# Kernel optimization log

Hardware: AMD Instinct MI355X
Metric: run time of the kernel (lower is better)

## Reference

```python
import jax, jax.numpy as jnp
import numpy as np


def conv3d(x, w, b, pad):
    # x: (B,C,D,H,W), w: (O,I,kd,kh,kw)
    y = jax.lax.conv_general_dilated(
        x, w, window_strides=(1, 1, 1), padding=[(pad, pad)] * 3,
        dimension_numbers=('NCDHW', 'OIDHW', 'NCDHW'))
    return y + b[None, :, None, None, None]


def setup_inputs() -> dict:
    key = jax.random.key(0)
    ks = jax.random.split(key, 8)
    B, C, D, H, W = 8, 128, 16, 32, 32
    C8 = C // 8
    return {
        'x': jax.random.normal(ks[0], (B, C, D, H, W), dtype=jnp.float32),
        'gamma': jax.random.normal(ks[1], (1,), dtype=jnp.float32),
        'w_k': jax.random.normal(ks[2], (C8, C, 1, 1, 1), dtype=jnp.float32) * 0.05,
        'b_k': jax.random.normal(ks[3], (C8,), dtype=jnp.float32) * 0.05,
        'w_q': jax.random.normal(ks[4], (C8, C, 1, 1, 1), dtype=jnp.float32) * 0.05,
        'b_q': jax.random.normal(ks[5], (C8,), dtype=jnp.float32) * 0.05,
        'w_v': jax.random.normal(ks[6], (C, C, 3, 3, 3), dtype=jnp.float32) * 0.02,
        'b_v': jax.random.normal(ks[7], (C,), dtype=jnp.float32) * 0.05,
    }


def reference(x, gamma, w_k, b_k, w_q, b_q, w_v, b_v):
    B, C, D, H, W = x.shape
    HW = H * W
    k = conv3d(x, w_k, b_k, 0)   # (B, C/8, D, H, W)
    q = conv3d(x, w_q, b_q, 0)   # (B, C/8, D, H, W)
    v = conv3d(x, w_v, b_v, 1)   # (B, C, D, H, W)

    # --- spatial (P) attention over HW positions, feature dim (C/8)*D ---
    kf = k.reshape(B, -1, HW)
    qf = q.reshape(B, -1, HW)
    # cor[b,s,t] = sum_f k[b,f,s] q[b,f,t]; softmax over t
    A_p = jax.nn.softmax(jnp.einsum('bfs,bft->bst', kf, qf), axis=-1)  # (B,HW,HW)
    vf = v.reshape(B, C * D, HW)
    # Patt[b,m,j] = sum_t v[b,m,t] A_p[b,j,t]  (v @ A_p^T)
    Patt = jnp.einsum('bmt,bjt->bmj', vf, A_p).reshape(B, C, D, H, W)

    # --- depth (D) attention over D slices, feature dim (C/8)*H*W ---
    kd = k.transpose(0, 2, 1, 3, 4).reshape(B, D, -1)
    qd = q.transpose(0, 2, 1, 3, 4).reshape(B, D, -1)
    A_d = jax.nn.softmax(jnp.einsum('bdf,bef->bde', kd, qd), axis=-1)  # (B,D,D)
    vd = v.transpose(0, 2, 1, 3, 4).reshape(B, D, -1)  # (B, D, C*H*W)
    # Datt[b,j,f] = sum_d A_d[b,j,d] vd[b,d,f]
    Datt = jnp.einsum('bjd,bdf->bjf', A_d, vd).reshape(B, D, C, H, W)
    Datt = Datt.transpose(0, 2, 1, 3, 4)  # (B,C,D,H,W)

    return gamma[0] * (Patt + Datt) + x
```

## Files before the change

kernel.cpp:

```cpp
#include <hip/hip_runtime.h>

#define HW   1024
#define DHW  16384

typedef __attribute__((ext_vector_type(8))) short short8;
typedef __attribute__((ext_vector_type(4))) float f32x4;

static __device__ __forceinline__ ushort f2bf(float f) {
  unsigned u = __float_as_uint(f);
  unsigned r = (u + 0x7fffu + ((u >> 16) & 1u)) >> 16;
  return (ushort)r;
}
static __device__ __forceinline__ float bf2f(ushort u) {
  return __uint_as_float(((unsigned)u) << 16);
}
static __device__ __forceinline__ void async_copy16(const ushort* g, ushort* l) {
  __builtin_amdgcn_global_load_lds(
      (const __attribute__((address_space(1))) unsigned int*)g,
      (__attribute__((address_space(3))) unsigned int*)l, 16, 0, 0);
}

__global__ __launch_bounds__(256) void kq_kernel(
    const float* __restrict__ x, const float* __restrict__ wk,
    const float* __restrict__ bk, const float* __restrict__ wq,
    const float* __restrict__ bq, float* __restrict__ k, float* __restrict__ q,
    ushort* __restrict__ xt) {
  __shared__ float wks[16 * 128];
  __shared__ float wqs[16 * 128];
  int tid = threadIdx.x;
  for (int i = tid; i < 2048; i += 256) { wks[i] = wk[i]; wqs[i] = wq[i]; }
  __syncthreads();
  int b = blockIdx.y;
  int p = blockIdx.x * 256 + tid;
  int z = p >> 10, hw = p & 1023;
  float ak[16], aq[16];
#pragma unroll
  for (int o = 0; o < 16; ++o) { ak[o] = 0.f; aq[o] = 0.f; }
  const float* xb = x + (size_t)b * 128 * DHW + p;
  ushort* xtp = xt + (((size_t)(b * 16 + z) * 16) * 1024 + hw) * 8;
  for (int chunk = 0; chunk < 16; ++chunk) {
    ushort pack[8];
#pragma unroll
    for (int c8 = 0; c8 < 8; ++c8) {
      int c = chunk * 8 + c8;
      float xv = xb[(size_t)c * DHW];
      pack[c8] = f2bf(xv);
#pragma unroll
      for (int o = 0; o < 16; ++o) {
        ak[o] += wks[o * 128 + c] * xv;
        aq[o] += wqs[o * 128 + c] * xv;
      }
    }
    *(uint4*)&xtp[(size_t)chunk * 1024 * 8] = *(const uint4*)pack;
  }
#pragma unroll
  for (int o = 0; o < 16; ++o) {
    k[((size_t)b * 16 + o) * DHW + p] = ak[o] + bk[o];
    q[((size_t)b * 16 + o) * DHW + p] = aq[o] + bq[o];
  }
}

__global__ __launch_bounds__(256) void wprep_kernel(
    const float* __restrict__ wv, ushort* __restrict__ wt,
    ushort* __restrict__ zbuf) {
  if (blockIdx.x == 0 && threadIdx.x < 512) zbuf[threadIdx.x] = 0;
  int i = blockIdx.x * 256 + threadIdx.x;
  if (i >= 27 * 128 * 128) return;
  int c8 = i & 7;
  int t = i >> 3;
  int o = t & 127; t >>= 7;
  int tap = t % 9; t /= 9;
  int chunk = t & 15;
  int kd = t >> 4;
  wt[i] = f2bf(wv[(size_t)(o * 128 + chunk * 8 + c8) * 27 + kd * 9 + tap]);
}

__global__ __launch_bounds__(256, 2) void vconv_mfma_kernel(
    const ushort* __restrict__ xt, const ushort* __restrict__ wt,
    const float* __restrict__ bv, const ushort* __restrict__ zbuf,
    ushort* __restrict__ v) {
  __shared__ __align__(16) ushort xs[1536 * 8];
  __shared__ __align__(16) ushort wsm[2304 * 8];
  int tid = threadIdx.x;
  int wave = tid >> 6;
  int ml = tid & 15;
  int quad = (tid >> 4) & 3;
  int bz = blockIdx.x;
  int b = bz & 7, z = bz >> 3;
  int h0 = blockIdx.y * 8;
  int o0 = blockIdx.z * 64;

  f32x4 acc[4][4];
#pragma unroll
  for (int s = 0; s < 4; ++s)
#pragma unroll
    for (int t = 0; t < 4; ++t) acc[s][t] = (f32x4){0.f, 0.f, 0.f, 0.f};

  int cb0[4];
#pragma unroll
  for (int t = 0; t < 4; ++t)
    cb0[t] = (wave * 2 + (t >> 1)) * 34 + (t & 1) * 16 + ml;

  int xoff[6]; bool okx[6];
#pragma unroll
  for (int it = 0; it < 6; ++it) {
    int i = it * 256 + tid;
    int cu = i / 340;
    int cell = i - cu * 340;
    int hr = cell / 34;
    int wc = cell - hr * 34;
    int h = h0 + hr - 1, ww = wc - 1;
    okx[it] = (i < 1360) && ((unsigned)h < 32u) && ((unsigned)ww < 32u);
    xoff[it] = cu * 1024 + h * 32 + ww;
  }
  int woff[9];
#pragma unroll
  for (int it = 0; it < 9; ++it) {
    int i = it * 256 + tid;
    int cu = i / 576;
    int r = i - cu * 576;
    int tap = r >> 6, ol = r & 63;
    woff[it] = (cu * 9 + tap) * 128 + o0 + ol;
  }

  const int KH[9] = {0, 0, 0, 1, 1, 1, 2, 2, 2};
  const int KW[9] = {0, 1, 2, 0, 1, 2, 0, 1, 2};

  for (int kd = 0; kd < 3; ++kd) {
    int zd = z + kd - 1;
    bool zok = (zd >= 0 && zd < 16);
    int zdc = zok ? zd : 0;
    const ushort* xbase = xt + (size_t)(b * 16 + zdc) * 16 * 1024 * 8;
    for (int cb = 0; cb < 4; ++cb) {
      const ushort* xsb = xbase + (size_t)cb * 4 * 1024 * 8;
      const ushort* wsb = wt + (size_t)(kd * 16 + cb * 4) * 9 * 128 * 8;
#pragma unroll
      for (int it = 0; it < 6; ++it) {
        const ushort* g = (zok && okx[it]) ? xsb + (size_t)xoff[it] * 8 : zbuf;
        async_copy16(g, &xs[(it * 256 + tid) * 8]);
      }
#pragma unroll
      for (int it = 0; it < 9; ++it)
        async_copy16(wsb + (size_t)woff[it] * 8, &wsm[(it * 256 + tid) * 8]);
      __syncthreads();
#pragma unroll
      for (int tap = 0; tap < 9; ++tap) {
        const int kh = KH[tap], kw = KW[tap];
        short8 af[4], bfr[4];
#pragma unroll
        for (int s = 0; s < 4; ++s)
          af[s] = *(const short8*)&wsm[(quad * 576 + tap * 64 + s * 16 + ml) * 8];
#pragma unroll
        for (int t = 0; t < 4; ++t) {
          int cell = cb0[t] + kh * 34 + kw;
          bfr[t] = *(const short8*)&xs[(quad * 340 + cell) * 8];
        }
#pragma unroll
        for (int s = 0; s < 4; ++s)
#pragma unroll
          for (int t = 0; t < 4; ++t)
            acc[s][t] = __builtin_amdgcn_mfma_f32_16x16x32_bf16(af[s], bfr[t], acc[s][t], 0, 0, 0);
      }
      __syncthreads();
    }
  }
#pragma unroll
  for (int s = 0; s < 4; ++s) {
    int o = o0 + s * 16 + quad * 4;
#pragma unroll
    for (int t = 0; t < 4; ++t) {
      int pl = wave * 64 + t * 16 + ml;
      ushort* dst = &v[((size_t)(b * 128 + o) * 16 + z) * 1024 + h0 * 32 + pl];
#pragma unroll
      for (int r = 0; r < 4; ++r)
        dst[(size_t)r * 16384] = f2bf(acc[s][t][r] + bv[o + r]);
    }
  }
}

__global__ __launch_bounds__(256) void kqt_kernel(
    const float* __restrict__ k, const float* __restrict__ q,
    ushort* __restrict__ kT, ushort* __restrict__ qT,
    float* __restrict__ rsum, float* __restrict__ Sd) {
  __shared__ __align__(16) ushort tile[32 * 264];
  int tid = threadIdx.x;
  int t0 = blockIdx.x;
  int b = blockIdx.y;
  if (t0 == 0) {
    *(float4*)&rsum[b * 1024 + tid * 4] = (float4){0.f, 0.f, 0.f, 0.f};
    Sd[b * 256 + tid] = 0.f;
  }
  int h0 = t0 * 32;

  {
    const float* s = k + (size_t)b * 16 * DHW;
    for (int it = 0; it < 32; ++it) {
      int i = it * 256 + tid;
      int oo = i >> 9, zz = (i >> 5) & 15, hl = i & 31;
      tile[hl * 264 + oo * 16 + zz] =
          f2bf(s[(size_t)oo * DHW + zz * 1024 + h0 + hl]);
    }
    __syncthreads();
    ushort* d = kT + ((size_t)b * 1024 + h0) * 256;
    for (int jt = 0; jt < 4; ++jt) {
      int j = jt * 256 + tid;
      int hl = j >> 5, c8 = (j & 31) * 8;
      *(uint4*)&d[(size_t)hl * 256 + c8] = *(const uint4*)&tile[hl * 264 + c8];
    }
    __syncthreads();
  }
  {
    const float* s = q + (size_t)b * 16 * DHW;
    for (int it = 0; it < 32; ++it) {
      int i = it * 256 + tid;
      int oo = i >> 9, zz = (i >> 5) & 15, hl = i & 31;
      tile[hl * 264 + oo * 16 + zz] =
          f2bf(s[(size_t)oo * DHW + zz * 1024 + h0 + hl]);
    }
    __syncthreads();
    ushort* d = qT + ((size_t)b * 1024 + h0) * 256;
    for (int jt = 0; jt < 4; ++jt) {
      int j = jt * 256 + tid;
      int hl = j >> 5, c8 = (j & 31) * 8;
      *(uint4*)&d[(size_t)hl * 256 + c8] = *(const uint4*)&tile[hl * 264 + c8];
    }
  }
}

__global__ __launch_bounds__(256, 2) void apx_kernel(
    const ushort* __restrict__ kT, const ushort* __restrict__ qT,
    ushort* __restrict__ A_p, float* __restrict__ rsum) {
  __shared__ __align__(16) ushort smem[32768];
  int tid = threadIdx.x;
  int wave = tid >> 6, lane = tid & 63;
  int ml = lane & 15, quad = lane >> 4;
  int wm = wave >> 1, wj = wave & 1;
  int b = blockIdx.x;
  int tile = blockIdx.y;
  int m0 = (tile >> 3) * 128;
  int j0 = (tile & 7) * 128;

  f32x4 acc[4][4];
#pragma unroll
  for (int s = 0; s < 4; ++s)
#pragma unroll
    for (int t = 0; t < 4; ++t) acc[s][t] = (f32x4){0.f, 0.f, 0.f, 0.f};

  const ushort* va = kT + ((size_t)b * 1024 + m0) * 256;
  const ushort* pa = qT + ((size_t)b * 1024 + j0) * 256;

  int srow[4], skc[4];
#pragma unroll
  for (int n = 0; n < 4; ++n) {
    int slot = wave * 256 + n * 64 + lane;
    srow[n] = slot >> 3;
    skc[n] = (slot & 7) ^ (srow[n] & 7);
  }

#pragma unroll
  for (int n = 0; n < 4; ++n) {
    async_copy16(va + (size_t)srow[n] * 256 + skc[n] * 8,
                 &smem[(wave * 256 + n * 64) * 8]);
    async_copy16(pa + (size_t)srow[n] * 256 + skc[n] * 8,
                 &smem[8192 + (wave * 256 + n * 64) * 8]);
  }
  __syncthreads();

  for (int t = 0; t < 4; ++t) {
    int cur = (t & 1) * 16384;
    int nxt = 16384 - cur;
    if (t < 3) {
      int kk = (t + 1) * 64;
#pragma unroll
      for (int n = 0; n < 4; ++n) {
        async_copy16(va + (size_t)srow[n] * 256 + kk + skc[n] * 8,
                     &smem[nxt + (wave * 256 + n * 64) * 8]);
        async_copy16(pa + (size_t)srow[n] * 256 + kk + skc[n] * 8,
                     &smem[nxt + 8192 + (wave * 256 + n * 64) * 8]);
      }
    }
#pragma unroll
    for (int ks = 0; ks < 2; ++ks) {
      short8 af[4], bfr[4];
#pragma unroll
      for (int s = 0; s < 4; ++s) {
        int row = wm * 64 + s * 16 + ml;
        int c = ks * 4 + quad;
        af[s] = *(const short8*)&smem[cur + (row * 8 + (c ^ (row & 7))) * 8];
      }
#pragma unroll
      for (int t2 = 0; t2 < 4; ++t2) {
        int row = wj * 64 + t2 * 16 + ml;
        int c = ks * 4 + quad;
        bfr[t2] = *(const short8*)&smem[cur + 8192 + (row * 8 + (c ^ (row & 7))) * 8];
      }
#pragma unroll
      for (int s = 0; s < 4; ++s)
#pragma unroll
        for (int t2 = 0; t2 < 4; ++t2)
          acc[s][t2] = __builtin_amdgcn_mfma_f32_16x16x32_bf16(af[s], bfr[t2], acc[s][t2], 0, 0, 0);
    }
    __syncthreads();
  }

#pragma unroll
  for (int s = 0; s < 4; ++s)
#pragma unroll
    for (int r = 0; r < 4; ++r) {
      float sum = 0.f;
#pragma unroll
      for (int t2 = 0; t2 < 4; ++t2) {
        float p = __expf(acc[s][t2][r]);
        acc[s][t2][r] = p;
        sum += p;
      }
      sum += __shfl_xor(sum, 1);
      sum += __shfl_xor(sum, 2);
      sum += __shfl_xor(sum, 4);
      sum += __shfl_xor(sum, 8);
      if (ml == 0) {
        int m = m0 + wm * 64 + s * 16 + quad * 4 + r;
        atomicAdd(&rsum[b * 1024 + m], sum);
      }
    }
#pragma unroll
  for (int s = 0; s < 4; ++s)
#pragma unroll
    for (int t2 = 0; t2 < 4; ++t2) {
      int j = j0 + wj * 64 + t2 * 16 + ml;
#pragma unroll
      for (int r = 0; r < 4; ++r) {
        int m = m0 + wm * 64 + s * 16 + quad * 4 + r;
        A_p[((size_t)b * 1024 + m) * 1024 + j] = f2bf(acc[s][t2][r]);
      }
    }
}

__global__ __launch_bounds__(256) void ad_part_kernel(
    const float* __restrict__ k, const float* __restrict__ q,
    float* __restrict__ Sd) {
  int tid = threadIdx.x;
  int b = blockIdx.x;
  int dj = blockIdx.y;
  int split = blockIdx.z;
  float acc[16];
#pragma unroll
  for (int e = 0; e < 16; ++e) acc[e] = 0.f;
  const float* kb = k + (size_t)b * 256 * HW;
  const float* qb = q + (size_t)b * 256 * HW;
  int fend = (split + 1) * 4096;
  for (int f = split * 4096 + tid; f < fend; f += 256) {
    int oc = f >> 10, hw = f & 1023;
    float kv = kb[(oc * 16 + dj) * HW + hw];
#pragma unroll
    for (int e = 0; e < 16; ++e)
      acc[e] += kv * qb[(oc * 16 + e) * HW + hw];
  }
  int lane = tid & 63;
#pragma unroll
  for (int e = 0; e < 16; ++e) {
    float s = acc[e];
    for (int off = 32; off >= 1; off >>= 1) s += __shfl_xor(s, off);
    if (lane == 0) atomicAdd(&Sd[b * 256 + dj * 16 + e], s);
  }
}

__global__ __launch_bounds__(128) void ad_fin_kernel(
    const float* __restrict__ Sd, float* __restrict__ A_d) {
  int t = threadIdx.x;
  const float* row = Sd + (size_t)t * 16;
  float m = row[0];
#pragma unroll
  for (int e = 1; e < 16; ++e) m = fmaxf(m, row[e]);
  float p[16], s = 0.f;
#pragma unroll
  for (int e = 0; e < 16; ++e) { p[e] = __expf(row[e] - m); s += p[e]; }
  float inv = 1.f / s;
#pragma unroll
  for (int e = 0; e < 16; ++e) A_d[(size_t)t * 16 + e] = p[e] * inv;
}

__global__ __launch_bounds__(256, 2) void combine_mfma_kernel(
    const ushort* __restrict__ vb, const ushort* __restrict__ apb,
    const float* __restrict__ A_d, const float* __restrict__ rsum,
    const float* __restrict__ x, const float* __restrict__ gamma,
    float* __restrict__ out) {
  __shared__ __align__(16) ushort smem[32768];
  __shared__ float Adt[272];
  int tid = threadIdx.x;
  int wave = tid >> 6, lane = tid & 63;
  int ml = lane & 15, quad = lane >> 4;
  int wm = wave >> 1, wj = wave & 1;
  int b = blockIdx.x;
  int tile = blockIdx.y;
  int m0 = (tile >> 3) * 128;
  int j0 = (tile & 7) * 128;
  Adt[(tid & 15) * 17 + (tid >> 4)] = A_d[b * 256 + tid];

  f32x4 acc[4][4];
#pragma unroll
  for (int s = 0; s < 4; ++s)
#pragma unroll
    for (int t = 0; t < 4; ++t) acc[s][t] = (f32x4){0.f, 0.f, 0.f, 0.f};

  const ushort* va = vb + ((size_t)b * 2048 + m0) * 1024;
  const ushort* pa = apb + ((size_t)b * 1024 + j0) * 1024;

  int srow[4], skc[4];
#pragma unroll
  for (int n = 0; n < 4; ++n) {
    int slot = wave * 256 + n * 64 + lane;
    srow[n] = slot >> 3;
    skc[n] = (slot & 7) ^ (srow[n] & 7);
  }

#pragma unroll
  for (int n = 0; n < 4; ++n) {
    async_copy16(va + (size_t)srow[n] * 1024 + skc[n] * 8,
                 &smem[(wave * 256 + n * 64) * 8]);
    async_copy16(pa + (size_t)srow[n] * 1024 + skc[n] * 8,
                 &smem[8192 + (wave * 256 + n * 64) * 8]);
  }
  __syncthreads();

  for (int t = 0; t < 16; ++t) {
    int cur = (t & 1) * 16384;
    int nxt = 16384 - cur;
    if (t < 15) {
      int kk = (t + 1) * 64;
#pragma unroll
      for (int n = 0; n < 4; ++n) {
        async_copy16(va + (size_t)srow[n] * 1024 + kk + skc[n] * 8,
                     &smem[nxt + (wave * 256 + n * 64) * 8]);
        async_copy16(pa + (size_t)srow[n] * 1024 + kk + skc[n] * 8,
                     &smem[nxt + 8192 + (wave * 256 + n * 64) * 8]);
      }
    }
#pragma unroll
    for (int ks = 0; ks < 2; ++ks) {
      short8 af[4], bfr[4];
#pragma unroll
      for (int s = 0; s < 4; ++s) {
        int row = wm * 64 + s * 16 + ml;
        int c = ks * 4 + quad;
        af[s] = *(const short8*)&smem[cur + (row * 8 + (c ^ (row & 7))) * 8];
      }
#pragma unroll
      for (int t2 = 0; t2 < 4; ++t2) {
        int row = wj * 64 + t2 * 16 + ml;
        int c = ks * 4 + quad;
        bfr[t2] = *(const short8*)&smem[cur + 8192 + (row * 8 + (c ^ (row & 7))) * 8];
      }
#pragma unroll
      for (int s = 0; s < 4; ++s)
#pragma unroll
        for (int t2 = 0; t2 < 4; ++t2)
          acc[s][t2] = __builtin_amdgcn_mfma_f32_16x16x32_bf16(af[s], bfr[t2], acc[s][t2], 0, 0, 0);
    }
    __syncthreads();
  }

  float invr[4];
#pragma unroll
  for (int t2 = 0; t2 < 4; ++t2)
    invr[t2] = 1.f / rsum[b * 1024 + j0 + wj * 64 + t2 * 16 + ml];
#pragma unroll
  for (int s = 0; s < 4; ++s)
#pragma unroll
    for (int t2 = 0; t2 < 4; ++t2)
#pragma unroll
      for (int r = 0; r < 4; ++r) acc[s][t2][r] *= invr[t2];

  for (int i = tid; i < 2048; i += 256) {
    int row = i >> 4, jc = i & 15;
    uint4 val = *(const uint4*)&vb[((size_t)b * 2048 + m0 + row) * 1024 + j0 + jc * 8];
    *(uint4*)&smem[row * 136 + jc * 8] = val;
  }
  __syncthreads();

#pragma unroll
  for (int d = 0; d < 16; ++d) {
    float ar[4];
#pragma unroll
    for (int r = 0; r < 4; ++r) ar[r] = Adt[d * 17 + quad * 4 + r];
#pragma unroll
    for (int s = 0; s < 4; ++s) {
      const ushort* vrow = &smem[(wm * 64 + s * 16 + d) * 136];
#pragma unroll
      for (int t2 = 0; t2 < 4; ++t2) {
        float vv = bf2f(vrow[wj * 64 + t2 * 16 + ml]);
#pragma unroll
        for (int r = 0; r < 4; ++r) acc[s][t2][r] += ar[r] * vv;
      }
    }
  }

  float g = gamma[0];
#pragma unroll
  for (int s = 0; s < 4; ++s) {
#pragma unroll
    for (int t2 = 0; t2 < 4; ++t2) {
      int jrel = wj * 64 + t2 * 16 + ml;
#pragma unroll
      for (int r = 0; r < 4; ++r) {
        int m = m0 + wm * 64 + s * 16 + quad * 4 + r;
        size_t idx = ((size_t)b * 2048 + m) * 1024 + j0 + jrel;
        out[idx] = g * acc[s][t2][r] + x[idx];
      }
    }
  }
}

extern "C" void kernel_launch(void* const* d_in, const int* in_sizes, int n_in,
                              void* d_out, int out_size, void* d_ws, size_t ws_size,
                              hipStream_t stream) {
  const float* x     = (const float*)d_in[0];
  const float* gamma = (const float*)d_in[1];
  const float* w_k   = (const float*)d_in[2];
  const float* b_k   = (const float*)d_in[3];
  const float* w_q   = (const float*)d_in[4];
  const float* b_q   = (const float*)d_in[5];
  const float* w_v   = (const float*)d_in[6];
  const float* b_v   = (const float*)d_in[7];
  float* out = (float*)d_out;

  float* k    = (float*)d_ws;
  float* q    = k + 2097152;
  float* A_d  = q + 2097152;
  ushort* vbf = (ushort*)(A_d + 2048);
  ushort* apb = vbf + 16777216;
  ushort* wt  = apb + 8388608;
  ushort* zbuf = wt + 442368;
  ushort* xt  = zbuf + 512;
  ushort* kT16 = xt;
  ushort* qT16 = xt + 2097152;
  float* rsum  = (float*)(xt + 4194304);
  float* Sd    = rsum + 8192;

  wprep_kernel<<<dim3(1728), 256, 0, stream>>>(w_v, wt, zbuf);
  kq_kernel<<<dim3(64, 8), 256, 0, stream>>>(x, w_k, b_k, w_q, b_q, k, q, xt);
  vconv_mfma_kernel<<<dim3(128, 4, 2), 256, 0, stream>>>(xt, wt, b_v, zbuf, vbf);
  kqt_kernel<<<dim3(32, 8), 256, 0, stream>>>(k, q, kT16, qT16, rsum, Sd);
  apx_kernel<<<dim3(8, 64), 256, 0, stream>>>(kT16, qT16, apb, rsum);
  ad_part_kernel<<<dim3(8, 16, 4), 256, 0, stream>>>(k, q, Sd);
  ad_fin_kernel<<<dim3(1), 128, 0, stream>>>(Sd, A_d);
  combine_mfma_kernel<<<dim3(8, 128), 256, 0, stream>>>(vbf, apb, A_d, rsum, x, gamma, out);
}
```

Baseline: 374.0 us.

## Merge small kernels to cut launch count and fold depth softmax into combine

Weight prep and the k/q projection now run in one launch, split by block index, and the kq weight smem layout is transposed so each channel's weights load as float4. The depth-attention partial sums run as extra blocks of the spatial attention kernel. The tiny depth softmax kernel is removed; each combine block recomputes the 16x16 softmax from Sd in shared memory. This removes several launches and serial gaps at the cost of redundant softmax work per block and mixed workloads within a grid. The Adt write by tid<16 relies on a later barrier in the main loop before Adt is read.

Result: faster. 333.2 us (-10.9%).

```diff
diff --git a/kernel.cpp b/kernel.cpp
--- a/kernel.cpp
+++ b/kernel.cpp
@@ -20,18 +20,37 @@
       (__attribute__((address_space(3))) unsigned int*)l, 16, 0, 0);
 }
 
-__global__ __launch_bounds__(256) void kq_kernel(
+__global__ __launch_bounds__(256) void prep_kernel(
     const float* __restrict__ x, const float* __restrict__ wk,
     const float* __restrict__ bk, const float* __restrict__ wq,
-    const float* __restrict__ bq, float* __restrict__ k, float* __restrict__ q,
-    ushort* __restrict__ xt) {
-  __shared__ float wks[16 * 128];
-  __shared__ float wqs[16 * 128];
+    const float* __restrict__ bq, const float* __restrict__ wv,
+    float* __restrict__ k, float* __restrict__ q,
+    ushort* __restrict__ xt, ushort* __restrict__ wt,
+    ushort* __restrict__ zbuf) {
+  __shared__ float wks[2048];
+  __shared__ float wqs[2048];
+  int gid = blockIdx.x;
   int tid = threadIdx.x;
-  for (int i = tid; i < 2048; i += 256) { wks[i] = wk[i]; wqs[i] = wq[i]; }
+  if (gid >= 512) {
+    if (gid == 512 && tid < 512) zbuf[tid] = 0;
+    int i = (gid - 512) * 256 + tid;
+    int c8 = i & 7;
+    int t = i >> 3;
+    int o = t & 127; t >>= 7;
+    int tap = t % 9; t /= 9;
+    int chunk = t & 15;
+    int kd = t >> 4;
+    wt[i] = f2bf(wv[(size_t)(o * 128 + chunk * 8 + c8) * 27 + kd * 9 + tap]);
+    return;
+  }
+  for (int i = tid; i < 2048; i += 256) {
+    int c = i >> 4, o = i & 15;
+    wks[i] = wk[o * 128 + c];
+    wqs[i] = wq[o * 128 + c];
+  }
   __syncthreads();
-  int b = blockIdx.y;
-  int p = blockIdx.x * 256 + tid;
+  int b = gid >> 6, bx = gid & 63;
+  int p = bx * 256 + tid;
   int z = p >> 10, hw = p & 1023;
   float ak[16], aq[16];
 #pragma unroll
@@ -45,10 +64,15 @@
       int c = chunk * 8 + c8;
       float xv = xb[(size_t)c * DHW];
       pack[c8] = f2bf(xv);
-#pragma unroll
-      for (int o = 0; o < 16; ++o) {
-        ak[o] += wks[o * 128 + c] * xv;
-        aq[o] += wqs[o * 128 + c] * xv;
+      const float4* wkc = (const float4*)&wks[c * 16];
+      const float4* wqc = (const float4*)&wqs[c * 16];
+#pragma unroll
+      for (int g = 0; g < 4; ++g) {
+        float4 wa = wkc[g], wb = wqc[g];
+        ak[g * 4 + 0] += wa.x * xv; ak[g * 4 + 1] += wa.y * xv;
+        ak[g * 4 + 2] += wa.z * xv; ak[g * 4 + 3] += wa.w * xv;
+        aq[g * 4 + 0] += wb.x * xv; aq[g * 4 + 1] += wb.y * xv;
+        aq[g * 4 + 2] += wb.z * xv; aq[g * 4 + 3] += wb.w * xv;
       }
     }
     *(uint4*)&xtp[(size_t)chunk * 1024 * 8] = *(const uint4*)pack;
@@ -58,21 +82,6 @@
     k[((size_t)b * 16 + o) * DHW + p] = ak[o] + bk[o];
     q[((size_t)b * 16 + o) * DHW + p] = aq[o] + bq[o];
   }
-}
-
-__global__ __launch_bounds__(256) void wprep_kernel(
-    const float* __restrict__ wv, ushort* __restrict__ wt,
-    ushort* __restrict__ zbuf) {
-  if (blockIdx.x == 0 && threadIdx.x < 512) zbuf[threadIdx.x] = 0;
-  int i = blockIdx.x * 256 + threadIdx.x;
-  if (i >= 27 * 128 * 128) return;
-  int c8 = i & 7;
-  int t = i >> 3;
-  int o = t & 127; t >>= 7;
-  int tap = t % 9; t /= 9;
-  int chunk = t & 15;
-  int kd = t >> 4;
-  wt[i] = f2bf(wv[(size_t)(o * 128 + chunk * 8 + c8) * 27 + kd * 9 + tap]);
 }
 
 __global__ __launch_bounds__(256, 2) void vconv_mfma_kernel(
@@ -227,16 +236,46 @@
   }
 }
 
-__global__ __launch_bounds__(256, 2) void apx_kernel(
+__global__ __launch_bounds__(256, 2) void att_kernel(
     const ushort* __restrict__ kT, const ushort* __restrict__ qT,
-    ushort* __restrict__ A_p, float* __restrict__ rsum) {
+    ushort* __restrict__ A_p, float* __restrict__ rsum,
+    const float* __restrict__ k, const float* __restrict__ q,
+    float* __restrict__ Sd) {
   __shared__ __align__(16) ushort smem[32768];
   int tid = threadIdx.x;
+  int b = blockIdx.x;
+  int by = blockIdx.y;
+
+  if (by >= 64) {
+    int t = by - 64;
+    int dj = t & 15, split = t >> 4;
+    float acc[16];
+#pragma unroll
+    for (int e = 0; e < 16; ++e) acc[e] = 0.f;
+    const float* kb = k + (size_t)b * 256 * HW;
+    const float* qb = q + (size_t)b * 256 * HW;
+    int fend = (split + 1) * 4096;
+    for (int f = split * 4096 + tid; f < fend; f += 256) {
+      int oc = f >> 10, hw = f & 1023;
+      float kv = kb[(oc * 16 + dj) * HW + hw];
+#pragma unroll
+      for (int e = 0; e < 16; ++e)
+        acc[e] += kv * qb[(oc * 16 + e) * HW + hw];
+    }
+    int lane = tid & 63;
+#pragma unroll
+    for (int e = 0; e < 16; ++e) {
+      float s = acc[e];
+      for (int off = 32; off >= 1; off >>= 1) s += __shfl_xor(s, off);
+      if (lane == 0) atomicAdd(&Sd[b * 256 + dj * 16 + e], s);
+    }
+    return;
+  }
+
   int wave = tid >> 6, lane = tid & 63;
   int ml = lane & 15, quad = lane >> 4;
   int wm = wave >> 1, wj = wave & 1;
-  int b = blockIdx.x;
-  int tile = blockIdx.y;
+  int tile = by;
   int m0 = (tile >> 3) * 128;
   int j0 = (tile & 7) * 128;
 
@@ -336,56 +375,13 @@
     }
 }
 
-__global__ __launch_bounds__(256) void ad_part_kernel(
-    const float* __restrict__ k, const float* __restrict__ q,
-    float* __restrict__ Sd) {
-  int tid = threadIdx.x;
-  int b = blockIdx.x;
-  int dj = blockIdx.y;
-  int split = blockIdx.z;
-  float acc[16];
-#pragma unroll
-  for (int e = 0; e < 16; ++e) acc[e] = 0.f;
-  const float* kb = k + (size_t)b * 256 * HW;
-  const float* qb = q + (size_t)b * 256 * HW;
-  int fend = (split + 1) * 4096;
-  for (int f = split * 4096 + tid; f < fend; f += 256) {
-    int oc = f >> 10, hw = f & 1023;
-    float kv = kb[(oc * 16 + dj) * HW + hw];
-#pragma unroll
-    for (int e = 0; e < 16; ++e)
-      acc[e] += kv * qb[(oc * 16 + e) * HW + hw];
-  }
-  int lane = tid & 63;
-#pragma unroll
-  for (int e = 0; e < 16; ++e) {
-    float s = acc[e];
-    for (int off = 32; off >= 1; off >>= 1) s += __shfl_xor(s, off);
-    if (lane == 0) atomicAdd(&Sd[b * 256 + dj * 16 + e], s);
-  }
-}
-
-__global__ __launch_bounds__(128) void ad_fin_kernel(
-    const float* __restrict__ Sd, float* __restrict__ A_d) {
-  int t = threadIdx.x;
-  const float* row = Sd + (size_t)t * 16;
-  float m = row[0];
-#pragma unroll
-  for (int e = 1; e < 16; ++e) m = fmaxf(m, row[e]);
-  float p[16], s = 0.f;
-#pragma unroll
-  for (int e = 0; e < 16; ++e) { p[e] = __expf(row[e] - m); s += p[e]; }
-  float inv = 1.f / s;
-#pragma unroll
-  for (int e = 0; e < 16; ++e) A_d[(size_t)t * 16 + e] = p[e] * inv;
-}
-
 __global__ __launch_bounds__(256, 2) void combine_mfma_kernel(
     const ushort* __restrict__ vb, const ushort* __restrict__ apb,
-    const float* __restrict__ A_d, const float* __restrict__ rsum,
+    const float* __restrict__ Sd, const float* __restrict__ rsum,
     const float* __restrict__ x, const float* __restrict__ gamma,
     float* __restrict__ out) {
   __shared__ __align__(16) ushort smem[32768];
+  __shared__ float Sdl[256];
   __shared__ float Adt[272];
   int tid = threadIdx.x;
   int wave = tid >> 6, lane = tid & 63;
@@ -395,7 +391,7 @@
   int tile = blockIdx.y;
   int m0 = (tile >> 3) * 128;
   int j0 = (tile & 7) * 128;
-  Adt[(tid & 15) * 17 + (tid >> 4)] = A_d[b * 256 + tid];
+  Sdl[tid] = Sd[b * 256 + tid];
 
   f32x4 acc[4][4];
 #pragma unroll
@@ -422,6 +418,18 @@
                  &smem[8192 + (wave * 256 + n * 64) * 8]);
   }
   __syncthreads();
+
+  if (tid < 16) {
+    float m = Sdl[tid * 16];
+#pragma unroll
+    for (int e = 1; e < 16; ++e) m = fmaxf(m, Sdl[tid * 16 + e]);
+    float p[16], s = 0.f;
+#pragma unroll
+    for (int e = 0; e < 16; ++e) { p[e] = __expf(Sdl[tid * 16 + e] - m); s += p[e]; }
+    float inv = 1.f / s;
+#pragma unroll
+    for (int e = 0; e < 16; ++e) Adt[e * 17 + tid] = p[e] * inv;
+  }
 
   for (int t = 0; t < 16; ++t) {
     int cur = (t & 1) * 16384;
@@ -537,12 +545,10 @@
   float* rsum  = (float*)(xt + 4194304);
   float* Sd    = rsum + 8192;
 
-  wprep_kernel<<<dim3(1728), 256, 0, stream>>>(w_v, wt, zbuf);
-  kq_kernel<<<dim3(64, 8), 256, 0, stream>>>(x, w_k, b_k, w_q, b_q, k, q, xt);
+  prep_kernel<<<dim3(2240), 256, 0, stream>>>(x, w_k, b_k, w_q, b_q, w_v,
+                                              k, q, xt, wt, zbuf);
   vconv_mfma_kernel<<<dim3(128, 4, 2), 256, 0, stream>>>(xt, wt, b_v, zbuf, vbf);
   kqt_kernel<<<dim3(32, 8), 256, 0, stream>>>(k, q, kT16, qT16, rsum, Sd);
-  apx_kernel<<<dim3(8, 64), 256, 0, stream>>>(kT16, qT16, apb, rsum);
-  ad_part_kernel<<<dim3(8, 16, 4), 256, 0, stream>>>(k, q, Sd);
-  ad_fin_kernel<<<dim3(1), 128, 0, stream>>>(Sd, A_d);
-  combine_mfma_kernel<<<dim3(8, 128), 256, 0, stream>>>(vbf, apb, A_d, rsum, x, gamma, out);
-}
+  att_kernel<<<dim3(8, 128), 256, 0, stream>>>(kT16, qT16, apb, rsum, k, q, Sd);
+  combine_mfma_kernel<<<dim3(8, 128), 256, 0, stream>>>(vbf, apb, Sd, rsum, x, gamma, out);
+}
```
